# Kernel optimization log

Measured on AMD Instinct MI355X. Metric: run time of the kernel, lower is better.

The kernel has to match this reference:

```python
import jax, jax.numpy as jnp
import numpy as np

B, T, K = 64, 4096, 48  # batch, seq_len, n_tags


def setup_inputs() -> dict:
    key = jax.random.key(0)
    k1, k2, k3 = jax.random.split(key, 3)
    labels = jax.random.randint(k1, (B, T), 0, K)
    y_true = jax.nn.one_hot(labels, K, dtype=jnp.float32)  # one-hot targets, per dense_loss docstring
    y_pred = jax.random.normal(k2, (B, T, K), dtype=jnp.float32)  # emission scores
    trans = jax.random.normal(k3, (K, K), dtype=jnp.float32) * 0.1  # transition matrix (glorot-ish scale)
    return {"y_true": y_true, "y_pred": y_pred, "trans": trans}


def reference(y_true, y_pred, trans):
    # mask: positions where all emission scores > -1e6 (padding marker)
    mask = jnp.all(y_pred > -1e6, axis=2, keepdims=True).astype(y_pred.dtype)  # (B,T,1)
    y_true = y_true * mask
    y_pred = y_pred * mask

    # target_score: per-label emission score + transition score of the true path
    point_score = jnp.einsum('bni,bni->b', y_true, y_pred)
    trans_score = jnp.einsum('bni,ij,bnj->b', y_true[:, :-1], trans, y_true[:, 1:])
    target = point_score + trans_score  # (B,)

    # log_norm_step recurrence (CRF forward algorithm), fused as a single scan
    init = y_pred[:, 0]  # (B,K)
    xs = jnp.swapaxes(y_pred[:, 1:], 0, 1)  # (T-1,B,K)
    ms = jnp.swapaxes(mask[:, 1:], 0, 1)    # (T-1,B,1)

    def step(s, xm):
        x, m = xm
        # logsumexp over previous-tag axis: s (B,K_prev) + trans (K_prev,K_cur)
        new = jax.scipy.special.logsumexp(s[:, :, None] + trans[None, :, :], axis=1) + x
        s = m * new + (1.0 - m) * s
        return s, None

    s_final, _ = jax.lax.scan(step, init, (xs, ms))
    log_norm = jax.scipy.special.logsumexp(s_final, axis=1)  # (B,)

    # dense_loss returns log_norm - target_score (negative log-likelihood per example)
    return log_norm - target
```

## Files before the change

kernel.cpp:

```cpp
#include <hip/hip_runtime.h>

#define BB 64
#define TT 4096
#define KK 48
#define UST 56
#define PST 56
#define WS_LS_OFF 16384
#define WS_U_OFF 32768
#define SEGBYTES 4608
#define SEGELEMS 2304

typedef __bf16 bf16_t;
typedef bf16_t bf16x8 __attribute__((ext_vector_type(8)));
typedef float f32x4 __attribute__((ext_vector_type(4)));
typedef float f32x16 __attribute__((ext_vector_type(16)));

__device__ __forceinline__ float fexp(float x) {
    return __builtin_amdgcn_exp2f(x * 1.4426950408889634f);
}
__device__ __forceinline__ float flog2(float x) { return __builtin_amdgcn_logf(x); }
__device__ __forceinline__ float rdlanef(float v, int l) {
    return __int_as_float(__builtin_amdgcn_readlane(__float_as_int(v), l));
}
__device__ __forceinline__ unsigned int bf16bits(float f) {
    return (unsigned int)__builtin_bit_cast(unsigned short, (bf16_t)f);
}
__device__ __forceinline__ float bf2f(bf16_t h) {
    return __uint_as_float(((unsigned int)__builtin_bit_cast(unsigned short, h)) << 16);
}
__device__ __forceinline__ unsigned int pktrunc(float lo, float hi) {
    return __builtin_amdgcn_perm(__float_as_uint(hi), __float_as_uint(lo), 0x07060302u);
}

__global__ __launch_bounds__(512, 4) void fused_kernel(
    const float* __restrict__ y_true, const float* __restrict__ y_pred,
    const float* __restrict__ trans, float* __restrict__ ws_target,
    int* __restrict__ ws_ls, bf16_t* __restrict__ ws_u, int nseg) {
    const int s = blockIdx.x, b = blockIdx.y;
    const int seglen = TT / nseg;
    const int nch_sub = seglen / 128;
    const int tid = threadIdx.x;
    const int w = tid >> 6;
    const int sub = w >> 2;
    const int wl = w & 3;
    const int lane = tid & 63;
    const int q = lane >> 4;
    const int n = lane & 15;
    const int ncol = 16 * wl + n;

    __shared__ __align__(16) float4 exf[2][64 * 13];
    __shared__ __align__(16) bf16_t Ubuf[2][48 * UST + 16];
    __shared__ unsigned long long pb[2];
    __shared__ int lsbA[4], lsbB[4];
    __shared__ float scpart[2];

    bf16x8 afrag[3][2];
    if (wl < 3) {
#pragma unroll
        for (int mt = 0; mt < 3; mt++) {
#pragma unroll
            for (int ks = 0; ks < 2; ks++) {
                bf16x8 f;
#pragma unroll
                for (int j = 0; j < 8; j++) {
                    int k = 32 * ks + 8 * q + j;
                    float v = (k < KK) ? fexp(trans[k * KK + 16 * mt + n]) : 0.0f;
                    f[j] = (bf16_t)v;
                }
                afrag[mt][ks] = f;
            }
        }
    }

    {
        uint4* p = (uint4*)&Ubuf[0][0];
        const int nq = 2 * (48 * UST + 16) / 8;
        for (int i = tid; i < nq; i += 512) p[i] = make_uint4(0, 0, 0, 0);
    }
    __syncthreads();
    if (tid < KK) {
        Ubuf[0][tid * UST + tid] = (bf16_t)1.0f;
        Ubuf[1][tid * UST + tid] = (bf16_t)1.0f;
    }

    const bf16_t* bptr0 = &Ubuf[sub][ncol * UST + 8 * q];
    const bf16_t* bptr1 = &Ubuf[sub][ncol * UST + 32 + 8 * q];
    bf16_t* wp0 = &Ubuf[sub][ncol * UST + 0 + 4 * q];
    bf16_t* wp1 = &Ubuf[sub][ncol * UST + 16 + 4 * q];
    bf16_t* wp2 = &Ubuf[sub][ncol * UST + 32 + 4 * q];

    f32x4 z4 = {0.0f, 0.0f, 0.0f, 0.0f};
    int ls = 0;
    int cnt = 0;
    float sc_acc = 0.0f;

    for (int ch = 0; ch < nch_sub; ch++) {
        __syncthreads();
        if (wl == 3) {
            const int gch = sub * nch_sub + ch;
            const int t0c = s * seglen + gch * 64;
            const size_t rowbase = ((size_t)b * TT + t0c + lane) * KK;
            const float4* yp4 = (const float4*)(y_pred + rowbase);
            const float4* yt4 = (const float4*)(y_true + rowbase);
            float dot = 0.0f, labf = 0.0f, pmin = 1e30f;
            float4* exrow = &exf[sub][lane * 13];
#pragma unroll 4
            for (int g = 0; g < 12; g++) {
                float4 p = yp4[g];
                float4 a = yt4[g];
                dot = fmaf(a.x, p.x, fmaf(a.y, p.y, fmaf(a.z, p.z, fmaf(a.w, p.w, dot))));
                float e0 = (float)(4 * g);
                labf = fmaf(a.x, e0, fmaf(a.y, e0 + 1.0f, fmaf(a.z, e0 + 2.0f, fmaf(a.w, e0 + 3.0f, labf))));
                pmin = fminf(pmin, fminf(fminf(p.x, p.y), fminf(p.z, p.w)));
                exrow[g] = make_float4(fexp(p.x), fexp(p.y), fexp(p.z), fexp(p.w));
            }
            bool mt_ok = pmin > -1e6f;
            unsigned long long bal = __ballot(mt_ok);
            if (lane == 0) pb[sub] = bal;

            float labB = 0.0f, pmB = 1e30f;
            const bool hasB = (t0c + 64 < TT);
            if (hasB && lane < 12) {
                const size_t bdbase = ((size_t)b * TT + t0c + 64) * KK;
                float4 a = ((const float4*)(y_true + bdbase))[lane];
                float4 p = ((const float4*)(y_pred + bdbase))[lane];
                float e0 = (float)(4 * lane);
                labB = fmaf(a.x, e0, fmaf(a.y, e0 + 1.0f, fmaf(a.z, e0 + 2.0f, a.w * (e0 + 3.0f))));
                pmB = fminf(fminf(p.x, p.y), fminf(p.z, p.w));
            }
#pragma unroll
            for (int off = 1; off < 16; off <<= 1) {
                labB += __shfl_xor(labB, off);
                pmB = fminf(pmB, __shfl_xor(pmB, off));
            }
            int labB_i = (int)(rdlanef(labB, 0) + 0.5f);
            float mB = (hasB && rdlanef(pmB, 0) > -1e6f) ? 1.0f : 0.0f;

            int labt = (int)(labf + 0.5f);
            float mft = mt_ok ? 1.0f : 0.0f;
            int lnx = __shfl(labt, (lane + 1) & 63);
            float mnx = __shfl(mft, (lane + 1) & 63);
            if (lane == 63) { lnx = labB_i; mnx = mB; }
            sc_acc += mft * dot + mft * mnx * trans[labt * KK + lnx];
        }
        __syncthreads();
        if (wl < 3) {
            const unsigned long long mk = pb[sub];
            const int tt0 = (s == 0 && sub == 0 && ch == 0) ? 1 : 0;
            for (int tt = tt0; tt < 64; tt++) {
                if (!((mk >> tt) & 1ull)) continue;

                bf16x8 bf0 = __builtin_bit_cast(bf16x8, *(const uint4*)bptr0);
                bf16x8 bf1 = __builtin_bit_cast(bf16x8, *(const uint4*)bptr1);

                f32x4 acc0 = __builtin_amdgcn_mfma_f32_16x16x32_bf16(afrag[0][0], bf0, z4, 0, 0, 0);
                acc0 = __builtin_amdgcn_mfma_f32_16x16x32_bf16(afrag[0][1], bf1, acc0, 0, 0, 0);
                f32x4 acc1 = __builtin_amdgcn_mfma_f32_16x16x32_bf16(afrag[1][0], bf0, z4, 0, 0, 0);
                acc1 = __builtin_amdgcn_mfma_f32_16x16x32_bf16(afrag[1][1], bf1, acc1, 0, 0, 0);
                f32x4 acc2 = __builtin_amdgcn_mfma_f32_16x16x32_bf16(afrag[2][0], bf0, z4, 0, 0, 0);
                acc2 = __builtin_amdgcn_mfma_f32_16x16x32_bf16(afrag[2][1], bf1, acc2, 0, 0, 0);

                if (++cnt >= 6) {
                    float v00 = rdlanef(acc0[0], 0);
                    int k = (int)(__float_as_uint(v00) >> 23) - 127;
                    float r = __uint_as_float((unsigned int)(127 - k) << 23);
                    ls += k;
                    cnt = 0;
                    float4 ex0 = exf[sub][tt * 13 + q];
                    ex0.x *= r; ex0.y *= r; ex0.z *= r; ex0.w *= r;
                    *(uint2*)wp0 = make_uint2(pktrunc(acc0[0] * ex0.x, acc0[1] * ex0.y),
                                              pktrunc(acc0[2] * ex0.z, acc0[3] * ex0.w));
                    float4 ex1 = exf[sub][tt * 13 + 4 + q];
                    ex1.x *= r; ex1.y *= r; ex1.z *= r; ex1.w *= r;
                    *(uint2*)wp1 = make_uint2(pktrunc(acc1[0] * ex1.x, acc1[1] * ex1.y),
                                              pktrunc(acc1[2] * ex1.z, acc1[3] * ex1.w));
                    float4 ex2 = exf[sub][tt * 13 + 8 + q];
                    ex2.x *= r; ex2.y *= r; ex2.z *= r; ex2.w *= r;
                    *(uint2*)wp2 = make_uint2(pktrunc(acc2[0] * ex2.x, acc2[1] * ex2.y),
                                              pktrunc(acc2[2] * ex2.z, acc2[3] * ex2.w));
                } else {
                    float4 ex0 = exf[sub][tt * 13 + q];
                    *(uint2*)wp0 = make_uint2(pktrunc(acc0[0] * ex0.x, acc0[1] * ex0.y),
                                              pktrunc(acc0[2] * ex0.z, acc0[3] * ex0.w));
                    float4 ex1 = exf[sub][tt * 13 + 4 + q];
                    *(uint2*)wp1 = make_uint2(pktrunc(acc1[0] * ex1.x, acc1[1] * ex1.y),
                                              pktrunc(acc1[2] * ex1.z, acc1[3] * ex1.w));
                    float4 ex2 = exf[sub][tt * 13 + 8 + q];
                    *(uint2*)wp2 = make_uint2(pktrunc(acc2[0] * ex2.x, acc2[1] * ex2.y),
                                              pktrunc(acc2[2] * ex2.z, acc2[3] * ex2.w));
                }
            }
        }
    }

    __syncthreads();
    if (sub == 1 && wl < 3 && lane == 0) lsbB[wl] = ls;
    if (wl == 3) {
#pragma unroll
        for (int off = 32; off; off >>= 1) sc_acc += __shfl_xor(sc_acc, off);
        if (lane == 0) scpart[sub] = sc_acc;
    }
    bf16_t* RB = (bf16_t*)&exf[1][0];
    __syncthreads();
    {
        uint4* rp = (uint4*)RB;
        for (int i = tid; i < 384; i += 512) rp[i] = make_uint4(0, 0, 0, 0);
    }
    __syncthreads();
    if (sub == 1 && wl < 3 && lane < KK) {
        const int dl = ls - lsbB[0];
        unsigned int wd[8];
#pragma unroll
        for (int j = 0; j < 8; j++) {
            float f0 = ldexpf(bf2f(Ubuf[1][(16 * wl + 2 * j) * UST + lane]), dl);
            float f1 = ldexpf(bf2f(Ubuf[1][(16 * wl + 2 * j + 1) * UST + lane]), dl);
            wd[j] = bf16bits(f0) | (bf16bits(f1) << 16);
        }
        *(uint4*)(RB + lane * 64 + 16 * wl) = make_uint4(wd[0], wd[1], wd[2], wd[3]);
        *(uint4*)(RB + lane * 64 + 16 * wl + 8) = make_uint4(wd[4], wd[5], wd[6], wd[7]);
    }
    __syncthreads();
    if (sub == 0 && wl < 3) {
        bf16x8 aB0, aB1, bf0, bf1;
        bf0 = __builtin_bit_cast(bf16x8, *(const uint4*)bptr0);
        bf1 = __builtin_bit_cast(bf16x8, *(const uint4*)bptr1);
        aB0 = __builtin_bit_cast(bf16x8, *(const uint4*)&RB[(16 * 0 + n) * 64 + 8 * q]);
        aB1 = __builtin_bit_cast(bf16x8, *(const uint4*)&RB[(16 * 0 + n) * 64 + 32 + 8 * q]);
        f32x4 acc0 = __builtin_amdgcn_mfma_f32_16x16x32_bf16(aB0, bf0, z4, 0, 0, 0);
        acc0 = __builtin_amdgcn_mfma_f32_16x16x32_bf16(aB1, bf1, acc0, 0, 0, 0);
        aB0 = __builtin_bit_cast(bf16x8, *(const uint4*)&RB[(16 * 1 + n) * 64 + 8 * q]);
        aB1 = __builtin_bit_cast(bf16x8, *(const uint4*)&RB[(16 * 1 + n) * 64 + 32 + 8 * q]);
        f32x4 acc1 = __builtin_amdgcn_mfma_f32_16x16x32_bf16(aB0, bf0, z4, 0, 0, 0);
        acc1 = __builtin_amdgcn_mfma_f32_16x16x32_bf16(aB1, bf1, acc1, 0, 0, 0);
        aB0 = __builtin_bit_cast(bf16x8, *(const uint4*)&RB[(16 * 2 + n) * 64 + 8 * q]);
        aB1 = __builtin_bit_cast(bf16x8, *(const uint4*)&RB[(16 * 2 + n) * 64 + 32 + 8 * q]);
        f32x4 acc2 = __builtin_amdgcn_mfma_f32_16x16x32_bf16(aB0, bf0, z4, 0, 0, 0);
        acc2 = __builtin_amdgcn_mfma_f32_16x16x32_bf16(aB1, bf1, acc2, 0, 0, 0);

        float v00 = rdlanef(acc0[0], 0);
        int k = (int)(__float_as_uint(v00) >> 23) - 127;
        float r = __uint_as_float((unsigned int)(127 - k) << 23);
        ls += k;
        *(uint2*)wp0 = make_uint2(pktrunc(acc0[0] * r, acc0[1] * r),
                                  pktrunc(acc0[2] * r, acc0[3] * r));
        *(uint2*)wp1 = make_uint2(pktrunc(acc1[0] * r, acc1[1] * r),
                                  pktrunc(acc1[2] * r, acc1[3] * r));
        *(uint2*)wp2 = make_uint2(pktrunc(acc2[0] * r, acc2[1] * r),
                                  pktrunc(acc2[2] * r, acc2[3] * r));
    }
    if (sub == 0 && wl < 3 && lane == 0) lsbA[wl] = ls;
    __syncthreads();
    if (sub == 0 && wl < 3 && lane < KK) {
        const int dl = ls - lsbA[0];
        bf16_t* Uo = ws_u + (size_t)(b * nseg + s) * SEGELEMS;
        unsigned int wd[8];
#pragma unroll
        for (int j = 0; j < 8; j++) {
            float f0 = ldexpf(bf2f(Ubuf[0][(16 * wl + 2 * j) * UST + lane]), dl);
            float f1 = ldexpf(bf2f(Ubuf[0][(16 * wl + 2 * j + 1) * UST + lane]), dl);
            wd[j] = bf16bits(f0) | (bf16bits(f1) << 16);
        }
        *(uint4*)(Uo + (size_t)lane * 48 + 16 * wl) = make_uint4(wd[0], wd[1], wd[2], wd[3]);
        *(uint4*)(Uo + (size_t)lane * 48 + 16 * wl + 8) = make_uint4(wd[4], wd[5], wd[6], wd[7]);
    }
    if (tid == 0) {
        ws_ls[b * nseg + s] = lsbA[0] + lsbB[0];
        ws_target[b * nseg + s] = scpart[0] + scpart[1];
    }
}

__device__ __forceinline__ int chain_product(const bf16_t* __restrict__ A, bf16_t* Ub, int lane) {
    const int half = lane >> 5;
    const int l31 = lane & 31;
    f32x16 z16;
#pragma unroll
    for (int r = 0; r < 16; r++) z16[r] = 0.0f;

    bf16x8 af[2][3];
#pragma unroll
    for (int mt = 0; mt < 2; mt++) {
        int m = l31 + 32 * mt;
#pragma unroll
        for (int ks = 0; ks < 3; ks++) {
            if (m < KK)
                af[mt][ks] = __builtin_bit_cast(bf16x8, *(const uint4*)&A[(size_t)m * 48 + 16 * ks + 8 * half]);
            else
                af[mt][ks] = __builtin_bit_cast(bf16x8, make_uint4(0, 0, 0, 0));
        }
    }
    bf16x8 bg[3][2];
#pragma unroll
    for (int ks = 0; ks < 3; ks++)
#pragma unroll
        for (int nt = 0; nt < 2; nt++)
            bg[ks][nt] = __builtin_bit_cast(bf16x8, *(const uint4*)&Ub[(l31 + 32 * nt) * PST + 16 * ks + 8 * half]);

    f32x16 acc[4];
#pragma unroll
    for (int mt = 0; mt < 2; mt++)
#pragma unroll
        for (int nt = 0; nt < 2; nt++) {
            f32x16 a0 = __builtin_amdgcn_mfma_f32_32x32x16_bf16(af[mt][0], bg[0][nt], z16, 0, 0, 0);
            a0 = __builtin_amdgcn_mfma_f32_32x32x16_bf16(af[mt][1], bg[1][nt], a0, 0, 0, 0);
            acc[mt * 2 + nt] = __builtin_amdgcn_mfma_f32_32x32x16_bf16(af[mt][2], bg[2][nt], a0, 0, 0, 0);
        }

    float v00 = rdlanef(acc[0][0], 0);
    int k = (int)(__float_as_uint(v00) >> 23) - 127;
    float r = __uint_as_float((unsigned int)(127 - k) << 23);

#pragma unroll
    for (int mt = 0; mt < 2; mt++)
#pragma unroll
        for (int nt = 0; nt < 2; nt++) {
            int c = l31 + 32 * nt;
#pragma unroll
            for (int g = 0; g < 4; g++) {
                int a0 = 32 * mt + 8 * g + 4 * half;
                if (a0 < KK) {
                    const f32x16& Aq = acc[mt * 2 + nt];
                    unsigned int u0 = bf16bits(Aq[4 * g + 0] * r) | (bf16bits(Aq[4 * g + 1] * r) << 16);
                    unsigned int u1 = bf16bits(Aq[4 * g + 2] * r) | (bf16bits(Aq[4 * g + 3] * r) << 16);
                    *(uint2*)&Ub[c * PST + a0] = make_uint2(u0, u1);
                }
            }
        }
    return k;
}

__device__ __forceinline__ int chain_product_ldsA(const bf16_t* As, bf16_t* Ub, int lane) {
    const int half = lane >> 5;
    const int l31 = lane & 31;
    f32x16 z16;
#pragma unroll
    for (int r = 0; r < 16; r++) z16[r] = 0.0f;

    bf16x8 af[2][3];
#pragma unroll
    for (int mt = 0; mt < 2; mt++) {
        int m = l31 + 32 * mt;
#pragma unroll
        for (int ks = 0; ks < 3; ks++) {
            bf16x8 f;
#pragma unroll
            for (int j = 0; j < 8; j++) {
                int k = 16 * ks + 8 * half + j;
                f[j] = (m < KK) ? As[k * PST + m] : (bf16_t)0.0f;
            }
            af[mt][ks] = f;
        }
    }
    bf16x8 bg[3][2];
#pragma unroll
    for (int ks = 0; ks < 3; ks++)
#pragma unroll
        for (int nt = 0; nt < 2; nt++)
            bg[ks][nt] = __builtin_bit_cast(bf16x8, *(const uint4*)&Ub[(l31 + 32 * nt) * PST + 16 * ks + 8 * half]);

    f32x16 acc[4];
#pragma unroll
    for (int mt = 0; mt < 2; mt++)
#pragma unroll
        for (int nt = 0; nt < 2; nt++) {
            f32x16 a0 = __builtin_amdgcn_mfma_f32_32x32x16_bf16(af[mt][0], bg[0][nt], z16, 0, 0, 0);
            a0 = __builtin_amdgcn_mfma_f32_32x32x16_bf16(af[mt][1], bg[1][nt], a0, 0, 0, 0);
            acc[mt * 2 + nt] = __builtin_amdgcn_mfma_f32_32x32x16_bf16(af[mt][2], bg[2][nt], a0, 0, 0, 0);
        }

    float v00 = rdlanef(acc[0][0], 0);
    int k = (int)(__float_as_uint(v00) >> 23) - 127;
    float r = __uint_as_float((unsigned int)(127 - k) << 23);

#pragma unroll
    for (int mt = 0; mt < 2; mt++)
#pragma unroll
        for (int nt = 0; nt < 2; nt++) {
            int c = l31 + 32 * nt;
#pragma unroll
            for (int g = 0; g < 4; g++) {
                int a0 = 32 * mt + 8 * g + 4 * half;
                if (a0 < KK) {
                    const f32x16& Aq = acc[mt * 2 + nt];
                    unsigned int u0 = bf16bits(Aq[4 * g + 0] * r) | (bf16bits(Aq[4 * g + 1] * r) << 16);
                    unsigned int u1 = bf16bits(Aq[4 * g + 2] * r) | (bf16bits(Aq[4 * g + 3] * r) << 16);
                    *(uint2*)&Ub[c * PST + a0] = make_uint2(u0, u1);
                }
            }
        }
    return k;
}

__global__ __launch_bounds__(256) void fold8_kernel(
    bf16_t* __restrict__ ws_u, int* __restrict__ ws_ls, int nseg) {
    const int s8 = blockIdx.x, b = blockIdx.y;
    const int tid = threadIdx.x;
    const int w = tid >> 6, lane = tid & 63;
    const int base = b * nseg + s8 * 8;

    __shared__ __align__(16) bf16_t Ws[4][64 * PST];
    __shared__ int lsp[8];

    {
        const bf16_t* sE = ws_u + (size_t)(base + 2 * w) * SEGELEMS;
        for (int k = 0; k < KK; k++)
            Ws[w][lane * PST + k] = (lane < KK) ? sE[(size_t)k * 48 + lane] : (bf16_t)0.0f;
        int lsk = ws_ls[base + 2 * w] + ws_ls[base + 2 * w + 1];
        lsk += chain_product(ws_u + (size_t)(base + 2 * w + 1) * SEGELEMS, Ws[w], lane);
        if (lane == 0) lsp[w] = lsk;
    }
    __syncthreads();
    int k1 = 0;
    if (w == 0) k1 = chain_product_ldsA(Ws[1], Ws[0], lane);
    if (w == 2) {
        int k2 = chain_product_ldsA(Ws[3], Ws[2], lane);
        if (lane == 0) lsp[5] = k2;
    }
    __syncthreads();
    if (w == 0) {
        int k3 = chain_product_ldsA(Ws[2], Ws[0], lane);
        if (lane < KK) {
            bf16_t* Uo = ws_u + (size_t)base * SEGELEMS;
            unsigned int wd[24];
#pragma unroll
            for (int j = 0; j < 24; j++) {
                unsigned int lo = (unsigned int)__builtin_bit_cast(unsigned short, Ws[0][(2 * j) * PST + lane]);
                unsigned int hi = (unsigned int)__builtin_bit_cast(unsigned short, Ws[0][(2 * j + 1) * PST + lane]);
                wd[j] = lo | (hi << 16);
            }
#pragma unroll
            for (int g = 0; g < 6; g++)
                *(uint4*)(Uo + (size_t)lane * 48 + 8 * g) =
                    make_uint4(wd[4 * g], wd[4 * g + 1], wd[4 * g + 2], wd[4 * g + 3]);
        }
        if (lane == 0)
            ws_ls[base] = lsp[0] + lsp[1] + lsp[2] + lsp[3] + k1 + lsp[5] + k3;
    }
}

__global__ __launch_bounds__(256) void final_kernel(
    const float* __restrict__ y_pred, const bf16_t* __restrict__ ws_u,
    const int* __restrict__ ws_ls, const float* __restrict__ ws_target,
    float* __restrict__ out, int nseg) {
    const int b = blockIdx.x;
    const int tid = threadIdx.x;
    const int w = tid >> 6, lane = tid & 63;
    const int npart = nseg / 8;

    __shared__ __align__(16) bf16_t Ws[4][64 * PST];
    __shared__ int lsp[8];
    if (tid < 8) lsp[tid] = 0;
    __syncthreads();

    if (2 * w < npart) {
        const int slotE = b * nseg + 16 * w;
        const int slotL = slotE + 8;
        const bf16_t* sE = ws_u + (size_t)slotE * SEGELEMS;
        for (int k = 0; k < KK; k++)
            Ws[w][lane * PST + k] = (lane < KK) ? sE[(size_t)k * 48 + lane] : (bf16_t)0.0f;
        int lsk = ws_ls[slotE] + ws_ls[slotL];
        lsk += chain_product(ws_u + (size_t)slotL * SEGELEMS, Ws[w], lane);
        if (lane == 0) lsp[w] = lsk;
    }
    __syncthreads();
    int k1 = 0;
    if (npart >= 4 && w == 0) k1 = chain_product_ldsA(Ws[1], Ws[0], lane);
    if (npart == 8 && w == 2) {
        int k2 = chain_product_ldsA(Ws[3], Ws[2], lane);
        if (lane == 0) lsp[5] = k2;
    }
    __syncthreads();

    if (w == 0) {
        int k3 = 0;
        if (npart == 8) k3 = chain_product_ldsA(Ws[2], Ws[0], lane);
        float L = (float)(lsp[0] + lsp[1] + lsp[2] + lsp[3] + k1 + lsp[5] + k3);

        float x0 = (lane < KK) ? y_pred[(size_t)b * TT * KK + lane] : 0.0f;
        bool ok0 = (lane >= KK) || (x0 > -1e6f);
        bool m0 = (__ballot(ok0) == ~0ull);
        float xeff = (lane < KK) ? (m0 ? x0 : 0.0f) : 0.0f;
        float c0 = rdlanef(xeff, 0);
        float q0 = (lane < KK) ? fexp(xeff - c0) : 0.0f;

        float p = 0.0f;
        if (lane < KK) {
            for (int c = 0; c < KK; c++) {
                float qc = rdlanef(q0, c);
                p = fmaf(bf2f(Ws[0][c * PST + lane]), qc, p);
            }
        }
#pragma unroll
        for (int off = 32; off; off >>= 1) p += __shfl_xor(p, off);

        float tg = (lane < nseg) ? ws_target[b * nseg + lane] : 0.0f;
#pragma unroll
        for (int off = 32; off; off >>= 1) tg += __shfl_xor(tg, off);

        if (lane == 0) {
            out[b] = c0 + 0.6931471805599453f * (L + flog2(p)) - tg;
        }
    }
}

extern "C" void kernel_launch(void* const* d_in, const int* in_sizes, int n_in,
                              void* d_out, int out_size, void* d_ws, size_t ws_size,
                              hipStream_t stream) {
    const float* y_true = (const float*)d_in[0];
    const float* y_pred = (const float*)d_in[1];
    const float* trans = (const float*)d_in[2];
    float* out = (float*)d_out;

    int nseg = 16;
    if (ws_size >= (size_t)WS_U_OFF + (size_t)BB * 32 * SEGBYTES) nseg = 32;

    float* ws_target = (float*)d_ws;
    int* ws_ls = (int*)((char*)d_ws + WS_LS_OFF);
    bf16_t* ws_u = (bf16_t*)((char*)d_ws + WS_U_OFF);

    fused_kernel<<<dim3(nseg, BB), 512, 0, stream>>>(
        y_true, y_pred, trans, ws_target, ws_ls, ws_u, nseg);
    fold8_kernel<<<dim3(nseg / 8, BB), 256, 0, stream>>>(ws_u, ws_ls, nseg);
    final_kernel<<<BB, 256, 0, stream>>>(y_pred, ws_u, ws_ls, ws_target, out, nseg);
}
```

Before: 258.5 us.

## Merge fold8 and final kernels into one fold-final kernel; raise occupancy hint

Removes the separate fold8 kernel. Each of four waves in the final kernel now folds nseg/4 consecutive segment matrices sequentially, then a tree combine finishes the job. This drops one kernel launch and a workspace round-trip. In exchange, per-wave serial chain products grow longer and run with less parallelism (64 blocks only). Also raises the fused_kernel launch_bounds min-blocks from 4 to 5, which may tighten the register budget.

```diff
diff --git a/kernel.cpp b/kernel.cpp
--- a/kernel.cpp
+++ b/kernel.cpp
@@ -32,7 +32,7 @@
     return __builtin_amdgcn_perm(__float_as_uint(hi), __float_as_uint(lo), 0x07060302u);
 }
 
-__global__ __launch_bounds__(512, 4) void fused_kernel(
+__global__ __launch_bounds__(512, 5) void fused_kernel(
     const float* __restrict__ y_true, const float* __restrict__ y_pred,
     const float* __restrict__ trans, float* __restrict__ ws_target,
     int* __restrict__ ws_ls, bf16_t* __restrict__ ws_u, int nseg) {
@@ -390,89 +390,43 @@
     return k;
 }
 
-__global__ __launch_bounds__(256) void fold8_kernel(
-    bf16_t* __restrict__ ws_u, int* __restrict__ ws_ls, int nseg) {
-    const int s8 = blockIdx.x, b = blockIdx.y;
-    const int tid = threadIdx.x;
-    const int w = tid >> 6, lane = tid & 63;
-    const int base = b * nseg + s8 * 8;
-
-    __shared__ __align__(16) bf16_t Ws[4][64 * PST];
-    __shared__ int lsp[8];
-
-    {
-        const bf16_t* sE = ws_u + (size_t)(base + 2 * w) * SEGELEMS;
-        for (int k = 0; k < KK; k++)
-            Ws[w][lane * PST + k] = (lane < KK) ? sE[(size_t)k * 48 + lane] : (bf16_t)0.0f;
-        int lsk = ws_ls[base + 2 * w] + ws_ls[base + 2 * w + 1];
-        lsk += chain_product(ws_u + (size_t)(base + 2 * w + 1) * SEGELEMS, Ws[w], lane);
-        if (lane == 0) lsp[w] = lsk;
-    }
-    __syncthreads();
-    int k1 = 0;
-    if (w == 0) k1 = chain_product_ldsA(Ws[1], Ws[0], lane);
-    if (w == 2) {
-        int k2 = chain_product_ldsA(Ws[3], Ws[2], lane);
-        if (lane == 0) lsp[5] = k2;
-    }
-    __syncthreads();
-    if (w == 0) {
-        int k3 = chain_product_ldsA(Ws[2], Ws[0], lane);
-        if (lane < KK) {
-            bf16_t* Uo = ws_u + (size_t)base * SEGELEMS;
-            unsigned int wd[24];
-#pragma unroll
-            for (int j = 0; j < 24; j++) {
-                unsigned int lo = (unsigned int)__builtin_bit_cast(unsigned short, Ws[0][(2 * j) * PST + lane]);
-                unsigned int hi = (unsigned int)__builtin_bit_cast(unsigned short, Ws[0][(2 * j + 1) * PST + lane]);
-                wd[j] = lo | (hi << 16);
-            }
-#pragma unroll
-            for (int g = 0; g < 6; g++)
-                *(uint4*)(Uo + (size_t)lane * 48 + 8 * g) =
-                    make_uint4(wd[4 * g], wd[4 * g + 1], wd[4 * g + 2], wd[4 * g + 3]);
-        }
-        if (lane == 0)
-            ws_ls[base] = lsp[0] + lsp[1] + lsp[2] + lsp[3] + k1 + lsp[5] + k3;
-    }
-}
-
-__global__ __launch_bounds__(256) void final_kernel(
+__global__ __launch_bounds__(256) void fold_final_kernel(
     const float* __restrict__ y_pred, const bf16_t* __restrict__ ws_u,
     const int* __restrict__ ws_ls, const float* __restrict__ ws_target,
     float* __restrict__ out, int nseg) {
     const int b = blockIdx.x;
     const int tid = threadIdx.x;
     const int w = tid >> 6, lane = tid & 63;
-    const int npart = nseg / 8;
+    const int per = nseg / 4;
 
     __shared__ __align__(16) bf16_t Ws[4][64 * PST];
     __shared__ int lsp[8];
     if (tid < 8) lsp[tid] = 0;
     __syncthreads();
 
-    if (2 * w < npart) {
-        const int slotE = b * nseg + 16 * w;
-        const int slotL = slotE + 8;
-        const bf16_t* sE = ws_u + (size_t)slotE * SEGELEMS;
+    {
+        const int base = b * nseg + per * w;
+        const bf16_t* s0 = ws_u + (size_t)base * SEGELEMS;
         for (int k = 0; k < KK; k++)
-            Ws[w][lane * PST + k] = (lane < KK) ? sE[(size_t)k * 48 + lane] : (bf16_t)0.0f;
-        int lsk = ws_ls[slotE] + ws_ls[slotL];
-        lsk += chain_product(ws_u + (size_t)slotL * SEGELEMS, Ws[w], lane);
+            Ws[w][lane * PST + k] = (lane < KK) ? s0[(size_t)k * 48 + lane] : (bf16_t)0.0f;
+        int lsk = ws_ls[base];
+        for (int j = 1; j < per; j++) {
+            lsk += ws_ls[base + j];
+            lsk += chain_product(ws_u + (size_t)(base + j) * SEGELEMS, Ws[w], lane);
+        }
         if (lane == 0) lsp[w] = lsk;
     }
     __syncthreads();
     int k1 = 0;
-    if (npart >= 4 && w == 0) k1 = chain_product_ldsA(Ws[1], Ws[0], lane);
-    if (npart == 8 && w == 2) {
+    if (w == 0) k1 = chain_product_ldsA(Ws[1], Ws[0], lane);
+    if (w == 2) {
         int k2 = chain_product_ldsA(Ws[3], Ws[2], lane);
         if (lane == 0) lsp[5] = k2;
     }
     __syncthreads();
 
     if (w == 0) {
-        int k3 = 0;
-        if (npart == 8) k3 = chain_product_ldsA(Ws[2], Ws[0], lane);
+        int k3 = chain_product_ldsA(Ws[2], Ws[0], lane);
         float L = (float)(lsp[0] + lsp[1] + lsp[2] + lsp[3] + k1 + lsp[5] + k3);
 
         float x0 = (lane < KK) ? y_pred[(size_t)b * TT * KK + lane] : 0.0f;
@@ -519,6 +473,5 @@
 
     fused_kernel<<<dim3(nseg, BB), 512, 0, stream>>>(
         y_true, y_pred, trans, ws_target, ws_ls, ws_u, nseg);
-    fold8_kernel<<<dim3(nseg / 8, BB), 256, 0, stream>>>(ws_u, ws_ls, nseg);
-    final_kernel<<<BB, 256, 0, stream>>>(y_pred, ws_u, ws_ls, ws_target, out, nseg);
-}
+    fold_final_kernel<<<BB, 256, 0, stream>>>(y_pred, ws_u, ws_ls, ws_target, out, nseg);
+}
```

Measured after the change: 257.6 us. About the same (-0.3%).
